# Kernel optimization log

Hardware: AMD Instinct MI355X
Metric: run time of the kernel (lower is better)

Reference implementation:

```python
import jax, jax.numpy as jnp
import numpy as np

SEQ_LEN = 180
LATENT = 128
HIDDEN = 256
BATCH = 8192


def setup_inputs() -> dict:
    key = jax.random.key(0)
    ks = jax.random.split(key, 9)
    s = 1.0 / np.sqrt(HIDDEN)
    return {
        "z": jax.random.normal(ks[0], (BATCH, LATENT), jnp.float32),
        "fc_w": jax.random.normal(ks[1], (HIDDEN, LATENT), jnp.float32) * (1.0 / np.sqrt(LATENT)),
        "fc_b": jax.random.normal(ks[2], (HIDDEN,), jnp.float32) * 0.1,
        "w_ih": jax.random.normal(ks[3], (3 * HIDDEN, 2), jnp.float32) * s,
        "b_ih": jax.random.normal(ks[4], (3 * HIDDEN,), jnp.float32) * s,
        "w_hh": jax.random.normal(ks[5], (3 * HIDDEN, HIDDEN), jnp.float32) * s,
        "b_hh": jax.random.normal(ks[6], (3 * HIDDEN,), jnp.float32) * s,
        "out_w": jax.random.normal(ks[7], (2, HIDDEN), jnp.float32) * s,
        "out_b": jax.random.normal(ks[8], (2,), jnp.float32) * 0.1,
    }


def reference(z, fc_w, fc_b, w_ih, b_ih, w_hh, b_hh, out_w, out_b):
    # h0 = tanh(fc(z))  -> [B, H]
    h0 = jnp.tanh(z @ fc_w.T + fc_b)
    B = z.shape[0]
    # GRU input is all-zeros, so input-hidden gates are a constant bias: [B, 3H]
    gi = jnp.zeros((B, 2), z.dtype) @ w_ih.T + b_ih
    gi_r, gi_z, gi_n = jnp.split(gi, 3, axis=-1)

    def step(h, _):
        gh = h @ w_hh.T + b_hh                 # [B, 3H]
        gh_r, gh_z, gh_n = jnp.split(gh, 3, axis=-1)
        r = jax.nn.sigmoid(gi_r + gh_r)
        zg = jax.nn.sigmoid(gi_z + gh_z)
        n = jnp.tanh(gi_n + r * gh_n)
        h_new = (1.0 - zg) * n + zg * h
        return h_new, h_new

    _, hs = jax.lax.scan(step, h0, None, length=SEQ_LEN)  # [T, B, H]
    hs = jnp.swapaxes(hs, 0, 1)                            # [B, T, H]
    return hs @ out_w.T + out_b                            # [B, T, 2]
```

## Files before the change

### kernel.cpp

```cpp
#include <hip/hip_runtime.h>
#include <hip/hip_bf16.h>

#define T_SEQ  180
#define LATENT 128
#define HIDDEN 256

typedef __attribute__((ext_vector_type(8))) short  short8;
typedef __attribute__((ext_vector_type(4))) float  floatx4;
typedef __attribute__((ext_vector_type(4))) int    intx4;

#define WQ_OFF    0
#define FCW_OFF   196608
#define SCW_OFF   262144
#define OUTW_OFF  265216
#define SWOUT_OFF 269312

#define H8_STRIDE  272
#define H8B_OFF    8704
#define OBUF_OFF   17408
#define SMEM_BYTES 19456

__device__ __forceinline__ unsigned short f2bf(float f) {
    unsigned int u = __float_as_uint(f);
    u += 0x7fffu + ((u >> 16) & 1u);
    return (unsigned short)(u >> 16);
}

__device__ __forceinline__ float sigmoid_fast(float x) {
    return __builtin_amdgcn_rcpf(1.0f + __expf(-x));
}
__device__ __forceinline__ float tanh_fast(float x) {
    return 1.0f - 2.0f * __builtin_amdgcn_rcpf(1.0f + __expf(2.0f * x));
}

__global__ void pack_scales(const float* __restrict__ whh, float* __restrict__ scales) {
    int wid  = blockIdx.x * 4 + (threadIdx.x >> 6);
    int lane = threadIdx.x & 63;
    const float* src = whh + (size_t)wid * 256 + lane * 4;
    float m = 0.0f;
#pragma unroll
    for (int j = 0; j < 4; ++j) m = fmaxf(m, fabsf(src[j]));
#pragma unroll
    for (int d = 1; d < 64; d <<= 1) m = fmaxf(m, __shfl_xor(m, d, 64));
    if (lane == 0) scales[wid] = m;
}

__global__ void pack_whh_i8(const float* __restrict__ whh, const float* __restrict__ scales,
                            signed char* __restrict__ dst) {
    int tid  = blockIdx.x * blockDim.x + threadIdx.x;
    int lane = tid & 63;
    int frag = tid >> 6;
    int kc   = frag & 3;
    int sub  = (frag >> 2) % 6;
    int w    = frag / 24;
    int g = sub >> 1, cs = sub & 1;
    int col  = w * 32 + cs * 16 + (lane & 15);
    int jout = g * 256 + col;
    int k0   = kc * 64 + ((lane >> 4) << 4);
    const float* src = whh + (size_t)jout * 256 + k0;
    float inv = 127.0f / scales[jout];
    signed char q[16];
#pragma unroll
    for (int j = 0; j < 16; ++j) {
        float v = __builtin_rintf(src[j] * inv);
        v = fminf(fmaxf(v, -127.0f), 127.0f);
        q[j] = (signed char)(int)v;
    }
    *(intx4*)(dst + (size_t)frag * 1024 + lane * 16) = *(intx4*)q;
}

__global__ void pack_fcw(const float* __restrict__ fcw, unsigned short* __restrict__ dst) {
    int tid  = blockIdx.x * blockDim.x + threadIdx.x;
    int lane = tid & 63;
    int frag = tid >> 6;
    int kc   = frag & 3;
    int cs   = (frag >> 2) & 1;
    int w    = frag >> 3;
    int col  = w * 32 + cs * 16 + (lane & 15);
    int k0   = kc * 32 + ((lane >> 4) << 3);
    const float* src = fcw + col * 128 + k0;
    unsigned int u[4];
#pragma unroll
    for (int j = 0; j < 4; ++j)
        u[j] = (unsigned int)f2bf(src[2 * j]) | ((unsigned int)f2bf(src[2 * j + 1]) << 16);
    *(uint4*)(dst + frag * 512 + lane * 8) = make_uint4(u[0], u[1], u[2], u[3]);
}

__global__ void pack_outw_i8(const float* __restrict__ out_w,
                             signed char* __restrict__ dst, float* __restrict__ swout) {
    __shared__ float sw[2];
    int tid = threadIdx.x;
    if (tid < 128) {
        int o = tid >> 6, lane = tid & 63;
        const float* src = out_w + o * 256 + lane * 4;
        float m = 0.0f;
#pragma unroll
        for (int j = 0; j < 4; ++j) m = fmaxf(m, fabsf(src[j]));
#pragma unroll
        for (int d = 1; d < 64; d <<= 1) m = fmaxf(m, __shfl_xor(m, d, 64));
        if (lane == 0) { sw[o] = m; swout[o] = m; }
    }
    __syncthreads();
    int sl = tid >> 6, lane = tid & 63;
    int n  = lane & 15;
    int k0 = sl * 64 + ((lane >> 4) << 4);
    signed char q[16];
#pragma unroll
    for (int j = 0; j < 16; ++j) {
        float v = 0.0f;
        if (n < 2) {
            v = __builtin_rintf(out_w[n * 256 + k0 + j] * (127.0f / sw[n]));
            v = fminf(fmaxf(v, -127.0f), 127.0f);
        }
        q[j] = (signed char)(int)v;
    }
    *(intx4*)(dst + sl * 1024 + lane * 16) = *(intx4*)q;
}

__global__ __launch_bounds__(512, 2) void gru_main(
    const float* __restrict__ z,
    const float* __restrict__ fc_b,
    const float* __restrict__ b_ih,
    const float* __restrict__ b_hh,
    const float* __restrict__ out_b,
    const unsigned char* __restrict__ ws,
    float* __restrict__ out)
{
    extern __shared__ unsigned char smem[];
    signed char* h8a  = (signed char*)smem;
    signed char* h8b  = (signed char*)(smem + H8B_OFF);
    float*       obuf = (float*)(smem + OBUF_OFF);

    const int tid  = threadIdx.x;
    const int lane = tid & 63;
    const int wv   = tid >> 6;
    const int l15  = lane & 15;
    const int qd   = lane >> 4;
    const int rh   = wv >> 2;
    const int sl   = wv & 3;
    const int rb   = blockIdx.x * 32;

    intx4 wq[24];
#pragma unroll
    for (int sub = 0; sub < 6; ++sub)
#pragma unroll
        for (int kc = 0; kc < 4; ++kc)
            wq[sub * 4 + kc] = *(const intx4*)(ws + WQ_OFF
                                + (size_t)((wv * 6 + sub) * 4 + kc) * 1024 + lane * 16);

    intx4 bproj = *(const intx4*)(ws + OUTW_OFF + sl * 1024 + lane * 16);
    const float* swout = (const float*)(ws + SWOUT_OFF);
    float psc = (l15 < 2) ? swout[l15] * (1.0f / 16129.0f) : 0.0f;

    const float* scales = (const float*)(ws + SCW_OFF);
    float cbr[2], cbz[2], bhn[2], bin[2], fcb[2], scq[3][2];
#pragma unroll
    for (int cs = 0; cs < 2; ++cs) {
        int col = wv * 32 + cs * 16 + l15;
        cbr[cs] = b_ih[col]       + b_hh[col];
        cbz[cs] = b_ih[256 + col] + b_hh[256 + col];
        bin[cs] = b_ih[512 + col];
        bhn[cs] = b_hh[512 + col];
        fcb[cs] = fc_b[col];
#pragma unroll
        for (int g = 0; g < 3; ++g)
            scq[g][cs] = scales[g * 256 + col] * (1.0f / 16129.0f);
    }
    float ob = (tid < 64) ? out_b[tid & 1] : 0.0f;

    floatx4 a0f[2][2];
#pragma unroll
    for (int rt = 0; rt < 2; ++rt)
#pragma unroll
        for (int cs = 0; cs < 2; ++cs)
            a0f[rt][cs] = (floatx4){0.f, 0.f, 0.f, 0.f};
#pragma unroll
    for (int kc = 0; kc < 4; ++kc) {
#pragma unroll
        for (int rt = 0; rt < 2; ++rt) {
            const float* zp = z + (size_t)(rb + rt * 16 + l15) * LATENT + kc * 32 + qd * 8;
            short8 afr;
#pragma unroll
            for (int j = 0; j < 8; ++j) afr[j] = (short)f2bf(zp[j]);
#pragma unroll
            for (int cs = 0; cs < 2; ++cs) {
                short8 bfr = *(const short8*)(ws + FCW_OFF
                                + (size_t)((wv * 2 + cs) * 4 + kc) * 1024 + lane * 16);
                a0f[rt][cs] = __builtin_amdgcn_mfma_f32_16x16x32_bf16(afr, bfr, a0f[rt][cs], 0, 0, 0);
            }
        }
    }

    float hm[2][2][4];
#pragma unroll
    for (int rt = 0; rt < 2; ++rt)
#pragma unroll
        for (int cs = 0; cs < 2; ++cs)
#pragma unroll
            for (int r = 0; r < 4; ++r) {
                float h = tanh_fast(a0f[rt][cs][r] + fcb[cs]);
                hm[rt][cs][r] = h;
                h8a[(rt * 16 + qd * 4 + r) * H8_STRIDE + wv * 32 + cs * 16 + l15] =
                    (signed char)(int)__builtin_rintf(h * 127.0f);
            }
    __syncthreads();

#pragma unroll 1
    for (int t = 0; t < T_SEQ; ++t) {
        const int p = t & 1;
        signed char* h8p = p ? h8b : h8a;
        signed char* h8n = p ? h8a : h8b;

        intx4 acc[2][6];
#pragma unroll
        for (int rt = 0; rt < 2; ++rt)
#pragma unroll
            for (int s = 0; s < 6; ++s) acc[rt][s] = (intx4){0, 0, 0, 0};
#pragma unroll
        for (int kc = 0; kc < 4; ++kc) {
            intx4 a80 = *(const intx4*)&h8p[(0  + l15) * H8_STRIDE + kc * 64 + qd * 16];
            intx4 a81 = *(const intx4*)&h8p[(16 + l15) * H8_STRIDE + kc * 64 + qd * 16];
#pragma unroll
            for (int s = 0; s < 6; ++s) {
                acc[0][s] = __builtin_amdgcn_mfma_i32_16x16x64_i8(a80, wq[s * 4 + kc], acc[0][s], 0, 0, 0);
                acc[1][s] = __builtin_amdgcn_mfma_i32_16x16x64_i8(a81, wq[s * 4 + kc], acc[1][s], 0, 0, 0);
            }
        }

        intx4 pj = (intx4){0, 0, 0, 0};
        {
            intx4 a8p = *(const intx4*)&h8p[(rh * 16 + l15) * H8_STRIDE + sl * 64 + qd * 16];
            pj = __builtin_amdgcn_mfma_i32_16x16x64_i8(a8p, bproj, pj, 0, 0, 0);
        }

        if (t >= 2 && tid < 64) {
            int rl = tid >> 1, o = tid & 1;
            int frh = rl >> 4, fr = rl & 15;
            int base = ((p ^ 1) * 2 + frh) * 128 + fr * 2 + o;
            float s = ob + obuf[base] + obuf[base + 32] + obuf[base + 64] + obuf[base + 96];
            out[(size_t)(rb + rl) * (T_SEQ * 2) + (t - 2) * 2 + o] = s;
        }

#pragma unroll
        for (int rt = 0; rt < 2; ++rt)
#pragma unroll
            for (int cs = 0; cs < 2; ++cs)
#pragma unroll
                for (int r = 0; r < 4; ++r) {
                    float xr = __builtin_fmaf((float)acc[rt][cs][r],     scq[0][cs], cbr[cs]);
                    float xz = __builtin_fmaf((float)acc[rt][2 + cs][r], scq[1][cs], cbz[cs]);
                    float xn = __builtin_fmaf((float)acc[rt][4 + cs][r], scq[2][cs], bhn[cs]);
                    float gr = sigmoid_fast(xr);
                    float gz = sigmoid_fast(xz);
                    float gn = tanh_fast(bin[cs] + gr * xn);
                    float h  = gn + gz * (hm[rt][cs][r] - gn);
                    hm[rt][cs][r] = h;
                    h8n[(rt * 16 + qd * 4 + r) * H8_STRIDE + wv * 32 + cs * 16 + l15] =
                        (signed char)(int)__builtin_rintf(h * 127.0f);
                }

        if (t >= 1 && l15 < 2) {
#pragma unroll
            for (int r = 0; r < 4; ++r)
                obuf[(p * 2 + rh) * 128 + sl * 32 + (qd * 4 + r) * 2 + l15] = (float)pj[r] * psc;
        }

        __syncthreads();
    }

    if (tid < 64) {
        int rl = tid >> 1, o = tid & 1;
        int frh = rl >> 4, fr = rl & 15;
        int base = (1 * 2 + frh) * 128 + fr * 2 + o;
        float s = ob + obuf[base] + obuf[base + 32] + obuf[base + 64] + obuf[base + 96];
        out[(size_t)(rb + rl) * (T_SEQ * 2) + 178 * 2 + o] = s;
    }
    {
        intx4 a8p = *(const intx4*)&h8a[(rh * 16 + l15) * H8_STRIDE + sl * 64 + qd * 16];
        intx4 pj = (intx4){0, 0, 0, 0};
        pj = __builtin_amdgcn_mfma_i32_16x16x64_i8(a8p, bproj, pj, 0, 0, 0);
        if (l15 < 2)
#pragma unroll
            for (int r = 0; r < 4; ++r)
                obuf[(0 * 2 + rh) * 128 + sl * 32 + (qd * 4 + r) * 2 + l15] = (float)pj[r] * psc;
    }
    __syncthreads();
    if (tid < 64) {
        int rl = tid >> 1, o = tid & 1;
        int frh = rl >> 4, fr = rl & 15;
        int base = (0 * 2 + frh) * 128 + fr * 2 + o;
        float s = ob + obuf[base] + obuf[base + 32] + obuf[base + 64] + obuf[base + 96];
        out[(size_t)(rb + rl) * (T_SEQ * 2) + 179 * 2 + o] = s;
    }
}

extern "C" void kernel_launch(void* const* d_in, const int* in_sizes, int n_in,
                              void* d_out, int out_size, void* d_ws, size_t ws_size,
                              hipStream_t stream) {
    const float* z     = (const float*)d_in[0];
    const float* fc_w  = (const float*)d_in[1];
    const float* fc_b  = (const float*)d_in[2];
    const float* b_ih  = (const float*)d_in[4];
    const float* w_hh  = (const float*)d_in[5];
    const float* b_hh  = (const float*)d_in[6];
    const float* out_w = (const float*)d_in[7];
    const float* out_b = (const float*)d_in[8];
    float* out = (float*)d_out;
    unsigned char* ws = (unsigned char*)d_ws;

    hipFuncSetAttribute((const void*)gru_main,
                        hipFuncAttributeMaxDynamicSharedMemorySize, SMEM_BYTES);

    pack_scales<<<192, 256, 0, stream>>>(w_hh, (float*)(ws + SCW_OFF));
    pack_whh_i8<<<48, 256, 0, stream>>>(w_hh, (const float*)(ws + SCW_OFF),
                                        (signed char*)(ws + WQ_OFF));
    pack_fcw<<<16, 256, 0, stream>>>(fc_w, (unsigned short*)(ws + FCW_OFF));
    pack_outw_i8<<<1, 256, 0, stream>>>(out_w, (signed char*)(ws + OUTW_OFF),
                                        (float*)(ws + SWOUT_OFF));
    gru_main<<<256, 512, SMEM_BYTES, stream>>>(z, fc_b, b_ih, b_hh, out_b, ws, out);
}
```

Before: 535.5 us.

## Halve rows per block, spill n-gate weights to LDS, fold log2e into constants

Each block now handles 16 batch rows instead of 32, so 512 blocks launch instead of 256. The n-gate W_hh fragments move from registers into a 64KB LDS region, which cuts the register footprint and lets launch bounds target 4 blocks per CU. The activations fold log2(e) into the precomputed biases and scales so they can call exp2 directly. The cost is extra LDS reads of weights on every timestep and half as many MFMAs per A-fragment load, traded for higher occupancy and a grid that spans more CUs.

```diff
diff --git a/kernel.cpp b/kernel.cpp
--- a/kernel.cpp
+++ b/kernel.cpp
@@ -8,6 +8,8 @@
 typedef __attribute__((ext_vector_type(8))) short  short8;
 typedef __attribute__((ext_vector_type(4))) float  floatx4;
 typedef __attribute__((ext_vector_type(4))) int    intx4;
+
+#define LOG2E 1.4426950408889634f
 
 #define WQ_OFF    0
 #define FCW_OFF   196608
@@ -15,10 +17,11 @@
 #define OUTW_OFF  265216
 #define SWOUT_OFF 269312
 
+#define H8A_OFF    65536
+#define H8B_OFF    69888
+#define OBUF_OFF   74240
+#define SMEM_BYTES 75264
 #define H8_STRIDE  272
-#define H8B_OFF    8704
-#define OBUF_OFF   17408
-#define SMEM_BYTES 19456
 
 __device__ __forceinline__ unsigned short f2bf(float f) {
     unsigned int u = __float_as_uint(f);
@@ -26,11 +29,12 @@
     return (unsigned short)(u >> 16);
 }
 
-__device__ __forceinline__ float sigmoid_fast(float x) {
-    return __builtin_amdgcn_rcpf(1.0f + __expf(-x));
-}
-__device__ __forceinline__ float tanh_fast(float x) {
-    return 1.0f - 2.0f * __builtin_amdgcn_rcpf(1.0f + __expf(2.0f * x));
+__device__ __forceinline__ float sig_e2(float ylog2e) {
+    return __builtin_amdgcn_rcpf(1.0f + __builtin_amdgcn_exp2f(-ylog2e));
+}
+__device__ __forceinline__ float tanh_e2(float y2log2e) {
+    return __builtin_fmaf(-2.0f,
+        __builtin_amdgcn_rcpf(1.0f + __builtin_amdgcn_exp2f(y2log2e)), 1.0f);
 }
 
 __global__ void pack_scales(const float* __restrict__ whh, float* __restrict__ scales) {
@@ -117,7 +121,7 @@
     *(intx4*)(dst + sl * 1024 + lane * 16) = *(intx4*)q;
 }
 
-__global__ __launch_bounds__(512, 2) void gru_main(
+__global__ __launch_bounds__(512, 4) void gru_main(
     const float* __restrict__ z,
     const float* __restrict__ fc_b,
     const float* __restrict__ b_ih,
@@ -127,7 +131,8 @@
     float* __restrict__ out)
 {
     extern __shared__ unsigned char smem[];
-    signed char* h8a  = (signed char*)smem;
+    signed char* wlds = (signed char*)smem;
+    signed char* h8a  = (signed char*)(smem + H8A_OFF);
     signed char* h8b  = (signed char*)(smem + H8B_OFF);
     float*       obuf = (float*)(smem + OBUF_OFF);
 
@@ -136,73 +141,76 @@
     const int wv   = tid >> 6;
     const int l15  = lane & 15;
     const int qd   = lane >> 4;
-    const int rh   = wv >> 2;
-    const int sl   = wv & 3;
-    const int rb   = blockIdx.x * 32;
-
-    intx4 wq[24];
-#pragma unroll
-    for (int sub = 0; sub < 6; ++sub)
+    const int rb   = blockIdx.x * 16;
+
+#pragma unroll
+    for (int s2 = 0; s2 < 2; ++s2)
+#pragma unroll
+        for (int kc = 0; kc < 4; ++kc) {
+            int gfrag = (wv * 6 + 4 + s2) * 4 + kc;
+            intx4 v = *(const intx4*)(ws + WQ_OFF + (size_t)gfrag * 1024 + lane * 16);
+            *(intx4*)(wlds + (wv * 8 + s2 * 4 + kc) * 1024 + lane * 16) = v;
+        }
+
+    intx4 wq[16];
+#pragma unroll
+    for (int sub = 0; sub < 4; ++sub)
 #pragma unroll
         for (int kc = 0; kc < 4; ++kc)
             wq[sub * 4 + kc] = *(const intx4*)(ws + WQ_OFF
                                 + (size_t)((wv * 6 + sub) * 4 + kc) * 1024 + lane * 16);
 
-    intx4 bproj = *(const intx4*)(ws + OUTW_OFF + sl * 1024 + lane * 16);
+    intx4 bproj = *(const intx4*)(ws + OUTW_OFF + (wv & 3) * 1024 + lane * 16);
     const float* swout = (const float*)(ws + SWOUT_OFF);
     float psc = (l15 < 2) ? swout[l15] * (1.0f / 16129.0f) : 0.0f;
 
     const float* scales = (const float*)(ws + SCW_OFF);
-    float cbr[2], cbz[2], bhn[2], bin[2], fcb[2], scq[3][2];
+    float cbrE[2], cbzE[2], bhnE2[2], binE2[2], fcbE2[2];
+    float scqrE[2], scqzE[2], scqnE2[2];
 #pragma unroll
     for (int cs = 0; cs < 2; ++cs) {
         int col = wv * 32 + cs * 16 + l15;
-        cbr[cs] = b_ih[col]       + b_hh[col];
-        cbz[cs] = b_ih[256 + col] + b_hh[256 + col];
-        bin[cs] = b_ih[512 + col];
-        bhn[cs] = b_hh[512 + col];
-        fcb[cs] = fc_b[col];
-#pragma unroll
-        for (int g = 0; g < 3; ++g)
-            scq[g][cs] = scales[g * 256 + col] * (1.0f / 16129.0f);
-    }
-    float ob = (tid < 64) ? out_b[tid & 1] : 0.0f;
-
-    floatx4 a0f[2][2];
-#pragma unroll
-    for (int rt = 0; rt < 2; ++rt)
-#pragma unroll
-        for (int cs = 0; cs < 2; ++cs)
-            a0f[rt][cs] = (floatx4){0.f, 0.f, 0.f, 0.f};
+        cbrE[cs]  = (b_ih[col]       + b_hh[col])       * LOG2E;
+        cbzE[cs]  = (b_ih[256 + col] + b_hh[256 + col]) * LOG2E;
+        binE2[cs] = b_ih[512 + col] * (2.0f * LOG2E);
+        bhnE2[cs] = b_hh[512 + col] * (2.0f * LOG2E);
+        fcbE2[cs] = fc_b[col] * (2.0f * LOG2E);
+        float s0 = scales[col]       * (1.0f / 16129.0f);
+        float s1 = scales[256 + col] * (1.0f / 16129.0f);
+        float s2 = scales[512 + col] * (1.0f / 16129.0f);
+        scqrE[cs]  = s0 * LOG2E;
+        scqzE[cs]  = s1 * LOG2E;
+        scqnE2[cs] = s2 * (2.0f * LOG2E);
+    }
+    float ob = out_b[tid & 1];
+
+    floatx4 a0f[2];
+#pragma unroll
+    for (int cs = 0; cs < 2; ++cs) a0f[cs] = (floatx4){0.f, 0.f, 0.f, 0.f};
 #pragma unroll
     for (int kc = 0; kc < 4; ++kc) {
-#pragma unroll
-        for (int rt = 0; rt < 2; ++rt) {
-            const float* zp = z + (size_t)(rb + rt * 16 + l15) * LATENT + kc * 32 + qd * 8;
-            short8 afr;
-#pragma unroll
-            for (int j = 0; j < 8; ++j) afr[j] = (short)f2bf(zp[j]);
-#pragma unroll
-            for (int cs = 0; cs < 2; ++cs) {
-                short8 bfr = *(const short8*)(ws + FCW_OFF
-                                + (size_t)((wv * 2 + cs) * 4 + kc) * 1024 + lane * 16);
-                a0f[rt][cs] = __builtin_amdgcn_mfma_f32_16x16x32_bf16(afr, bfr, a0f[rt][cs], 0, 0, 0);
-            }
-        }
-    }
-
-    float hm[2][2][4];
-#pragma unroll
-    for (int rt = 0; rt < 2; ++rt)
-#pragma unroll
-        for (int cs = 0; cs < 2; ++cs)
-#pragma unroll
-            for (int r = 0; r < 4; ++r) {
-                float h = tanh_fast(a0f[rt][cs][r] + fcb[cs]);
-                hm[rt][cs][r] = h;
-                h8a[(rt * 16 + qd * 4 + r) * H8_STRIDE + wv * 32 + cs * 16 + l15] =
-                    (signed char)(int)__builtin_rintf(h * 127.0f);
-            }
+        const float* zp = z + (size_t)(rb + l15) * LATENT + kc * 32 + qd * 8;
+        short8 afr;
+#pragma unroll
+        for (int j = 0; j < 8; ++j) afr[j] = (short)f2bf(zp[j]);
+#pragma unroll
+        for (int cs = 0; cs < 2; ++cs) {
+            short8 bfr = *(const short8*)(ws + FCW_OFF
+                            + (size_t)((wv * 2 + cs) * 4 + kc) * 1024 + lane * 16);
+            a0f[cs] = __builtin_amdgcn_mfma_f32_16x16x32_bf16(afr, bfr, a0f[cs], 0, 0, 0);
+        }
+    }
+
+    float hm[2][4];
+#pragma unroll
+    for (int cs = 0; cs < 2; ++cs)
+#pragma unroll
+        for (int r = 0; r < 4; ++r) {
+            float h = tanh_e2(__builtin_fmaf(a0f[cs][r], 2.0f * LOG2E, fcbE2[cs]));
+            hm[cs][r] = h;
+            h8a[(qd * 4 + r) * H8_STRIDE + wv * 32 + cs * 16 + l15] =
+                (signed char)(int)__builtin_rintf(h * 127.0f);
+        }
     __syncthreads();
 
 #pragma unroll 1
@@ -211,84 +219,78 @@
         signed char* h8p = p ? h8b : h8a;
         signed char* h8n = p ? h8a : h8b;
 
-        intx4 acc[2][6];
-#pragma unroll
-        for (int rt = 0; rt < 2; ++rt)
-#pragma unroll
-            for (int s = 0; s < 6; ++s) acc[rt][s] = (intx4){0, 0, 0, 0};
+        intx4 acc[6];
+#pragma unroll
+        for (int s = 0; s < 6; ++s) acc[s] = (intx4){0, 0, 0, 0};
 #pragma unroll
         for (int kc = 0; kc < 4; ++kc) {
-            intx4 a80 = *(const intx4*)&h8p[(0  + l15) * H8_STRIDE + kc * 64 + qd * 16];
-            intx4 a81 = *(const intx4*)&h8p[(16 + l15) * H8_STRIDE + kc * 64 + qd * 16];
-#pragma unroll
-            for (int s = 0; s < 6; ++s) {
-                acc[0][s] = __builtin_amdgcn_mfma_i32_16x16x64_i8(a80, wq[s * 4 + kc], acc[0][s], 0, 0, 0);
-                acc[1][s] = __builtin_amdgcn_mfma_i32_16x16x64_i8(a81, wq[s * 4 + kc], acc[1][s], 0, 0, 0);
-            }
+            intx4 a8 = *(const intx4*)&h8p[l15 * H8_STRIDE + kc * 64 + qd * 16];
+#pragma unroll
+            for (int s = 0; s < 4; ++s)
+                acc[s] = __builtin_amdgcn_mfma_i32_16x16x64_i8(a8, wq[s * 4 + kc], acc[s], 0, 0, 0);
+            intx4 bn0 = *(const intx4*)(wlds + (wv * 8 + 0 + kc) * 1024 + lane * 16);
+            intx4 bn1 = *(const intx4*)(wlds + (wv * 8 + 4 + kc) * 1024 + lane * 16);
+            acc[4] = __builtin_amdgcn_mfma_i32_16x16x64_i8(a8, bn0, acc[4], 0, 0, 0);
+            acc[5] = __builtin_amdgcn_mfma_i32_16x16x64_i8(a8, bn1, acc[5], 0, 0, 0);
         }
 
         intx4 pj = (intx4){0, 0, 0, 0};
-        {
-            intx4 a8p = *(const intx4*)&h8p[(rh * 16 + l15) * H8_STRIDE + sl * 64 + qd * 16];
+        if (wv < 4) {
+            intx4 a8p = *(const intx4*)&h8p[l15 * H8_STRIDE + (wv & 3) * 64 + qd * 16];
             pj = __builtin_amdgcn_mfma_i32_16x16x64_i8(a8p, bproj, pj, 0, 0, 0);
         }
 
-        if (t >= 2 && tid < 64) {
-            int rl = tid >> 1, o = tid & 1;
-            int frh = rl >> 4, fr = rl & 15;
-            int base = ((p ^ 1) * 2 + frh) * 128 + fr * 2 + o;
+        if (t >= 2 && tid >= 256 && tid < 288) {
+            int rl = (tid - 256) >> 1, o = tid & 1;
+            int base = (p ^ 1) * 128 + rl * 2 + o;
             float s = ob + obuf[base] + obuf[base + 32] + obuf[base + 64] + obuf[base + 96];
             out[(size_t)(rb + rl) * (T_SEQ * 2) + (t - 2) * 2 + o] = s;
         }
 
 #pragma unroll
-        for (int rt = 0; rt < 2; ++rt)
-#pragma unroll
-            for (int cs = 0; cs < 2; ++cs)
-#pragma unroll
-                for (int r = 0; r < 4; ++r) {
-                    float xr = __builtin_fmaf((float)acc[rt][cs][r],     scq[0][cs], cbr[cs]);
-                    float xz = __builtin_fmaf((float)acc[rt][2 + cs][r], scq[1][cs], cbz[cs]);
-                    float xn = __builtin_fmaf((float)acc[rt][4 + cs][r], scq[2][cs], bhn[cs]);
-                    float gr = sigmoid_fast(xr);
-                    float gz = sigmoid_fast(xz);
-                    float gn = tanh_fast(bin[cs] + gr * xn);
-                    float h  = gn + gz * (hm[rt][cs][r] - gn);
-                    hm[rt][cs][r] = h;
-                    h8n[(rt * 16 + qd * 4 + r) * H8_STRIDE + wv * 32 + cs * 16 + l15] =
-                        (signed char)(int)__builtin_rintf(h * 127.0f);
-                }
-
-        if (t >= 1 && l15 < 2) {
+        for (int cs = 0; cs < 2; ++cs)
+#pragma unroll
+            for (int r = 0; r < 4; ++r) {
+                float yr  = __builtin_fmaf((float)acc[cs][r],     scqrE[cs],  cbrE[cs]);
+                float yz  = __builtin_fmaf((float)acc[2 + cs][r], scqzE[cs],  cbzE[cs]);
+                float xn2 = __builtin_fmaf((float)acc[4 + cs][r], scqnE2[cs], bhnE2[cs]);
+                float gr = sig_e2(yr);
+                float gz = sig_e2(yz);
+                float gn = tanh_e2(__builtin_fmaf(gr, xn2, binE2[cs]));
+                float h  = __builtin_fmaf(gz, hm[cs][r] - gn, gn);
+                hm[cs][r] = h;
+                h8n[(qd * 4 + r) * H8_STRIDE + wv * 32 + cs * 16 + l15] =
+                    (signed char)(int)__builtin_rintf(h * 127.0f);
+            }
+
+        if (t >= 1 && wv < 4 && l15 < 2) {
 #pragma unroll
             for (int r = 0; r < 4; ++r)
-                obuf[(p * 2 + rh) * 128 + sl * 32 + (qd * 4 + r) * 2 + l15] = (float)pj[r] * psc;
+                obuf[p * 128 + (wv & 3) * 32 + (qd * 4 + r) * 2 + l15] = (float)pj[r] * psc;
         }
 
         __syncthreads();
     }
 
-    if (tid < 64) {
+    if (tid < 32) {
         int rl = tid >> 1, o = tid & 1;
-        int frh = rl >> 4, fr = rl & 15;
-        int base = (1 * 2 + frh) * 128 + fr * 2 + o;
+        int base = 128 + rl * 2 + o;
         float s = ob + obuf[base] + obuf[base + 32] + obuf[base + 64] + obuf[base + 96];
         out[(size_t)(rb + rl) * (T_SEQ * 2) + 178 * 2 + o] = s;
     }
-    {
-        intx4 a8p = *(const intx4*)&h8a[(rh * 16 + l15) * H8_STRIDE + sl * 64 + qd * 16];
+    if (wv < 4) {
+        intx4 a8p = *(const intx4*)&h8a[l15 * H8_STRIDE + (wv & 3) * 64 + qd * 16];
         intx4 pj = (intx4){0, 0, 0, 0};
         pj = __builtin_amdgcn_mfma_i32_16x16x64_i8(a8p, bproj, pj, 0, 0, 0);
         if (l15 < 2)
 #pragma unroll
             for (int r = 0; r < 4; ++r)
-                obuf[(0 * 2 + rh) * 128 + sl * 32 + (qd * 4 + r) * 2 + l15] = (float)pj[r] * psc;
+                obuf[(wv & 3) * 32 + (qd * 4 + r) * 2 + l15] = (float)pj[r] * psc;
     }
     __syncthreads();
-    if (tid < 64) {
+    if (tid < 32) {
         int rl = tid >> 1, o = tid & 1;
-        int frh = rl >> 4, fr = rl & 15;
-        int base = (0 * 2 + frh) * 128 + fr * 2 + o;
+        int base = rl * 2 + o;
         float s = ob + obuf[base] + obuf[base + 32] + obuf[base + 64] + obuf[base + 96];
         out[(size_t)(rb + rl) * (T_SEQ * 2) + 179 * 2 + o] = s;
     }
@@ -317,5 +319,5 @@
     pack_fcw<<<16, 256, 0, stream>>>(fc_w, (unsigned short*)(ws + FCW_OFF));
     pack_outw_i8<<<1, 256, 0, stream>>>(out_w, (signed char*)(ws + OUTW_OFF),
                                         (float*)(ws + SWOUT_OFF));
-    gru_main<<<256, 512, SMEM_BYTES, stream>>>(z, fc_b, b_ih, b_hh, out_b, ws, out);
-}
+    gru_main<<<512, 512, SMEM_BYTES, stream>>>(z, fc_b, b_ih, b_hh, out_b, ws, out);
+}
```

Result: faster. 512.6 us (-4.3%).

## Split GRU hidden columns across 16 waves and fold log2e into gate constants

Applied to the files above, without the earlier changes.

Each block now runs 1024 threads (16 waves). Every wave owns 16 hidden columns instead of 32, which halves the per-wave int8 weight registers and the gate math, so more waves can hide MFMA and transcendental latency within the serial time loop. Biases and scales are pre-multiplied by log2e so the gates use exp2 directly, saving a multiply per transcendental. The cost is more waves contending at each per-step __syncthreads, and the launch_bounds(1024,4) request may force register spilling.

```diff
diff --git a/kernel.cpp b/kernel.cpp
--- a/kernel.cpp
+++ b/kernel.cpp
@@ -8,6 +8,8 @@
 typedef __attribute__((ext_vector_type(8))) short  short8;
 typedef __attribute__((ext_vector_type(4))) float  floatx4;
 typedef __attribute__((ext_vector_type(4))) int    intx4;
+
+#define LOG2E 1.4426950408889634f
 
 #define WQ_OFF    0
 #define FCW_OFF   196608
@@ -26,11 +28,12 @@
     return (unsigned short)(u >> 16);
 }
 
-__device__ __forceinline__ float sigmoid_fast(float x) {
-    return __builtin_amdgcn_rcpf(1.0f + __expf(-x));
-}
-__device__ __forceinline__ float tanh_fast(float x) {
-    return 1.0f - 2.0f * __builtin_amdgcn_rcpf(1.0f + __expf(2.0f * x));
+__device__ __forceinline__ float sig_e2(float ylog2e) {
+    return __builtin_amdgcn_rcpf(1.0f + __builtin_amdgcn_exp2f(-ylog2e));
+}
+__device__ __forceinline__ float tanh_e2(float y2log2e) {
+    return __builtin_fmaf(-2.0f,
+        __builtin_amdgcn_rcpf(1.0f + __builtin_amdgcn_exp2f(y2log2e)), 1.0f);
 }
 
 __global__ void pack_scales(const float* __restrict__ whh, float* __restrict__ scales) {
@@ -117,7 +120,7 @@
     *(intx4*)(dst + sl * 1024 + lane * 16) = *(intx4*)q;
 }
 
-__global__ __launch_bounds__(512, 2) void gru_main(
+__global__ __launch_bounds__(1024, 4) void gru_main(
     const float* __restrict__ z,
     const float* __restrict__ fc_b,
     const float* __restrict__ b_ih,
@@ -134,75 +137,66 @@
     const int tid  = threadIdx.x;
     const int lane = tid & 63;
     const int wv   = tid >> 6;
+    const int cg   = wv;
     const int l15  = lane & 15;
     const int qd   = lane >> 4;
-    const int rh   = wv >> 2;
+    const int rh   = (wv >> 2) & 1;
     const int sl   = wv & 3;
     const int rb   = blockIdx.x * 32;
 
-    intx4 wq[24];
-#pragma unroll
-    for (int sub = 0; sub < 6; ++sub)
+    intx4 wq[12];
+#pragma unroll
+    for (int g = 0; g < 3; ++g)
 #pragma unroll
         for (int kc = 0; kc < 4; ++kc)
-            wq[sub * 4 + kc] = *(const intx4*)(ws + WQ_OFF
-                                + (size_t)((wv * 6 + sub) * 4 + kc) * 1024 + lane * 16);
+            wq[g * 4 + kc] = *(const intx4*)(ws + WQ_OFF
+                + (size_t)((((cg >> 1) * 6 + g * 2 + (cg & 1)) * 4 + kc)) * 1024 + lane * 16);
 
     intx4 bproj = *(const intx4*)(ws + OUTW_OFF + sl * 1024 + lane * 16);
     const float* swout = (const float*)(ws + SWOUT_OFF);
     float psc = (l15 < 2) ? swout[l15] * (1.0f / 16129.0f) : 0.0f;
 
     const float* scales = (const float*)(ws + SCW_OFF);
-    float cbr[2], cbz[2], bhn[2], bin[2], fcb[2], scq[3][2];
-#pragma unroll
-    for (int cs = 0; cs < 2; ++cs) {
-        int col = wv * 32 + cs * 16 + l15;
-        cbr[cs] = b_ih[col]       + b_hh[col];
-        cbz[cs] = b_ih[256 + col] + b_hh[256 + col];
-        bin[cs] = b_ih[512 + col];
-        bhn[cs] = b_hh[512 + col];
-        fcb[cs] = fc_b[col];
-#pragma unroll
-        for (int g = 0; g < 3; ++g)
-            scq[g][cs] = scales[g * 256 + col] * (1.0f / 16129.0f);
-    }
-    float ob = (tid < 64) ? out_b[tid & 1] : 0.0f;
-
-    floatx4 a0f[2][2];
-#pragma unroll
-    for (int rt = 0; rt < 2; ++rt)
-#pragma unroll
-        for (int cs = 0; cs < 2; ++cs)
-            a0f[rt][cs] = (floatx4){0.f, 0.f, 0.f, 0.f};
+    float cbrE, cbzE, bhnE2, binE2, fcbE2, scqrE, scqzE, scqnE2;
+    {
+        int col = cg * 16 + l15;
+        cbrE  = (b_ih[col]       + b_hh[col])       * LOG2E;
+        cbzE  = (b_ih[256 + col] + b_hh[256 + col]) * LOG2E;
+        binE2 = b_ih[512 + col] * (2.0f * LOG2E);
+        bhnE2 = b_hh[512 + col] * (2.0f * LOG2E);
+        fcbE2 = fc_b[col] * (2.0f * LOG2E);
+        scqrE  = scales[col]       * (LOG2E / 16129.0f);
+        scqzE  = scales[256 + col] * (LOG2E / 16129.0f);
+        scqnE2 = scales[512 + col] * (2.0f * LOG2E / 16129.0f);
+    }
+    float ob = out_b[tid & 1];
+
+    floatx4 a0f[2];
+#pragma unroll
+    for (int rt = 0; rt < 2; ++rt) a0f[rt] = (floatx4){0.f, 0.f, 0.f, 0.f};
 #pragma unroll
     for (int kc = 0; kc < 4; ++kc) {
+        short8 bfr = *(const short8*)(ws + FCW_OFF + (size_t)(cg * 4 + kc) * 1024 + lane * 16);
 #pragma unroll
         for (int rt = 0; rt < 2; ++rt) {
             const float* zp = z + (size_t)(rb + rt * 16 + l15) * LATENT + kc * 32 + qd * 8;
             short8 afr;
 #pragma unroll
             for (int j = 0; j < 8; ++j) afr[j] = (short)f2bf(zp[j]);
-#pragma unroll
-            for (int cs = 0; cs < 2; ++cs) {
-                short8 bfr = *(const short8*)(ws + FCW_OFF
-                                + (size_t)((wv * 2 + cs) * 4 + kc) * 1024 + lane * 16);
-                a0f[rt][cs] = __builtin_amdgcn_mfma_f32_16x16x32_bf16(afr, bfr, a0f[rt][cs], 0, 0, 0);
-            }
-        }
-    }
-
-    float hm[2][2][4];
+            a0f[rt] = __builtin_amdgcn_mfma_f32_16x16x32_bf16(afr, bfr, a0f[rt], 0, 0, 0);
+        }
+    }
+
+    float hm[2][4];
 #pragma unroll
     for (int rt = 0; rt < 2; ++rt)
 #pragma unroll
-        for (int cs = 0; cs < 2; ++cs)
-#pragma unroll
-            for (int r = 0; r < 4; ++r) {
-                float h = tanh_fast(a0f[rt][cs][r] + fcb[cs]);
-                hm[rt][cs][r] = h;
-                h8a[(rt * 16 + qd * 4 + r) * H8_STRIDE + wv * 32 + cs * 16 + l15] =
-                    (signed char)(int)__builtin_rintf(h * 127.0f);
-            }
+        for (int r = 0; r < 4; ++r) {
+            float h = tanh_e2(__builtin_fmaf(a0f[rt][r], 2.0f * LOG2E, fcbE2));
+            hm[rt][r] = h;
+            h8a[(rt * 16 + qd * 4 + r) * H8_STRIDE + cg * 16 + l15] =
+                (signed char)(int)__builtin_rintf(h * 127.0f);
+        }
     __syncthreads();
 
 #pragma unroll 1
@@ -211,32 +205,29 @@
         signed char* h8p = p ? h8b : h8a;
         signed char* h8n = p ? h8a : h8b;
 
-        intx4 acc[2][6];
-#pragma unroll
-        for (int rt = 0; rt < 2; ++rt)
-#pragma unroll
-            for (int s = 0; s < 6; ++s) acc[rt][s] = (intx4){0, 0, 0, 0};
+        intx4 acc[6];
+#pragma unroll
+        for (int s = 0; s < 6; ++s) acc[s] = (intx4){0, 0, 0, 0};
 #pragma unroll
         for (int kc = 0; kc < 4; ++kc) {
             intx4 a80 = *(const intx4*)&h8p[(0  + l15) * H8_STRIDE + kc * 64 + qd * 16];
             intx4 a81 = *(const intx4*)&h8p[(16 + l15) * H8_STRIDE + kc * 64 + qd * 16];
 #pragma unroll
-            for (int s = 0; s < 6; ++s) {
-                acc[0][s] = __builtin_amdgcn_mfma_i32_16x16x64_i8(a80, wq[s * 4 + kc], acc[0][s], 0, 0, 0);
-                acc[1][s] = __builtin_amdgcn_mfma_i32_16x16x64_i8(a81, wq[s * 4 + kc], acc[1][s], 0, 0, 0);
+            for (int g = 0; g < 3; ++g) {
+                acc[g]     = __builtin_amdgcn_mfma_i32_16x16x64_i8(a80, wq[g * 4 + kc], acc[g],     0, 0, 0);
+                acc[3 + g] = __builtin_amdgcn_mfma_i32_16x16x64_i8(a81, wq[g * 4 + kc], acc[3 + g], 0, 0, 0);
             }
         }
 
         intx4 pj = (intx4){0, 0, 0, 0};
-        {
+        if (wv < 8) {
             intx4 a8p = *(const intx4*)&h8p[(rh * 16 + l15) * H8_STRIDE + sl * 64 + qd * 16];
             pj = __builtin_amdgcn_mfma_i32_16x16x64_i8(a8p, bproj, pj, 0, 0, 0);
         }
 
-        if (t >= 2 && tid < 64) {
-            int rl = tid >> 1, o = tid & 1;
-            int frh = rl >> 4, fr = rl & 15;
-            int base = ((p ^ 1) * 2 + frh) * 128 + fr * 2 + o;
+        if (t >= 2 && tid >= 512 && tid < 576) {
+            int rl = (tid - 512) >> 1, o = tid & 1;
+            int base = ((p ^ 1) * 2 + (rl >> 4)) * 128 + (rl & 15) * 2 + o;
             float s = ob + obuf[base] + obuf[base + 32] + obuf[base + 64] + obuf[base + 96];
             out[(size_t)(rb + rl) * (T_SEQ * 2) + (t - 2) * 2 + o] = s;
         }
@@ -244,22 +235,20 @@
 #pragma unroll
         for (int rt = 0; rt < 2; ++rt)
 #pragma unroll
-            for (int cs = 0; cs < 2; ++cs)
-#pragma unroll
-                for (int r = 0; r < 4; ++r) {
-                    float xr = __builtin_fmaf((float)acc[rt][cs][r],     scq[0][cs], cbr[cs]);
-                    float xz = __builtin_fmaf((float)acc[rt][2 + cs][r], scq[1][cs], cbz[cs]);
-                    float xn = __builtin_fmaf((float)acc[rt][4 + cs][r], scq[2][cs], bhn[cs]);
-                    float gr = sigmoid_fast(xr);
-                    float gz = sigmoid_fast(xz);
-                    float gn = tanh_fast(bin[cs] + gr * xn);
-                    float h  = gn + gz * (hm[rt][cs][r] - gn);
-                    hm[rt][cs][r] = h;
-                    h8n[(rt * 16 + qd * 4 + r) * H8_STRIDE + wv * 32 + cs * 16 + l15] =
-                        (signed char)(int)__builtin_rintf(h * 127.0f);
-                }
-
-        if (t >= 1 && l15 < 2) {
+            for (int r = 0; r < 4; ++r) {
+                float yr  = __builtin_fmaf((float)acc[rt * 3 + 0][r], scqrE,  cbrE);
+                float yz  = __builtin_fmaf((float)acc[rt * 3 + 1][r], scqzE,  cbzE);
+                float xn2 = __builtin_fmaf((float)acc[rt * 3 + 2][r], scqnE2, bhnE2);
+                float gr = sig_e2(yr);
+                float gz = sig_e2(yz);
+                float gn = tanh_e2(__builtin_fmaf(gr, xn2, binE2));
+                float h  = __builtin_fmaf(gz, hm[rt][r] - gn, gn);
+                hm[rt][r] = h;
+                h8n[(rt * 16 + qd * 4 + r) * H8_STRIDE + cg * 16 + l15] =
+                    (signed char)(int)__builtin_rintf(h * 127.0f);
+            }
+
+        if (t >= 1 && wv < 8 && l15 < 2) {
 #pragma unroll
             for (int r = 0; r < 4; ++r)
                 obuf[(p * 2 + rh) * 128 + sl * 32 + (qd * 4 + r) * 2 + l15] = (float)pj[r] * psc;
@@ -270,12 +259,11 @@
 
     if (tid < 64) {
         int rl = tid >> 1, o = tid & 1;
-        int frh = rl >> 4, fr = rl & 15;
-        int base = (1 * 2 + frh) * 128 + fr * 2 + o;
+        int base = (1 * 2 + (rl >> 4)) * 128 + (rl & 15) * 2 + o;
         float s = ob + obuf[base] + obuf[base + 32] + obuf[base + 64] + obuf[base + 96];
         out[(size_t)(rb + rl) * (T_SEQ * 2) + 178 * 2 + o] = s;
     }
-    {
+    if (wv < 8) {
         intx4 a8p = *(const intx4*)&h8a[(rh * 16 + l15) * H8_STRIDE + sl * 64 + qd * 16];
         intx4 pj = (intx4){0, 0, 0, 0};
         pj = __builtin_amdgcn_mfma_i32_16x16x64_i8(a8p, bproj, pj, 0, 0, 0);
@@ -287,8 +275,7 @@
     __syncthreads();
     if (tid < 64) {
         int rl = tid >> 1, o = tid & 1;
-        int frh = rl >> 4, fr = rl & 15;
-        int base = (0 * 2 + frh) * 128 + fr * 2 + o;
+        int base = (0 * 2 + (rl >> 4)) * 128 + (rl & 15) * 2 + o;
         float s = ob + obuf[base] + obuf[base + 32] + obuf[base + 64] + obuf[base + 96];
         out[(size_t)(rb + rl) * (T_SEQ * 2) + 179 * 2 + o] = s;
     }
@@ -317,5 +304,5 @@
     pack_fcw<<<16, 256, 0, stream>>>(fc_w, (unsigned short*)(ws + FCW_OFF));
     pack_outw_i8<<<1, 256, 0, stream>>>(out_w, (signed char*)(ws + OUTW_OFF),
                                         (float*)(ws + SWOUT_OFF));
-    gru_main<<<256, 512, SMEM_BYTES, stream>>>(z, fc_b, b_ih, b_hh, out_b, ws, out);
-}
+    gru_main<<<256, 1024, SMEM_BYTES, stream>>>(z, fc_b, b_ih, b_hh, out_b, ws, out);
+}
```

Measured after the change: 480.1 us. 10.4% less time.
